# Optimization experiments

Hardware: AMD Instinct MI355X
Metric: run time of the kernel (lower is better)

Reference implementation:

```python
import jax, jax.numpy as jnp
import numpy as np

D = 64          # embed_dim
NH = 4          # nhead
DH = D // NH    # head dim
FF = 2048       # TransformerEncoderLayer default dim_feedforward
V = 1_000_000   # vocab (num items)
MAX_LEN = 50
INSERT_LEN = 10
EPS = 1e-5
N_LAYERS = 2


def setup_inputs() -> dict:
    key = jax.random.key(0)
    ks = jax.random.split(key, 8)
    s = 0.02
    return {
        "ht": jax.random.normal(ks[0], (D,), dtype=jnp.float32),
        "item_emb": jax.random.normal(ks[1], (V, D), dtype=jnp.float32) * s,
        "pos_emb": jax.random.normal(ks[2], (MAX_LEN, D), dtype=jnp.float32) * s,
        "in_proj_w": jax.random.normal(ks[3], (N_LAYERS, 3 * D, D), dtype=jnp.float32) * s,
        "in_proj_b": jnp.zeros((N_LAYERS, 3 * D), jnp.float32),
        "out_w": jax.random.normal(ks[4], (N_LAYERS, D, D), dtype=jnp.float32) * s,
        "out_b": jnp.zeros((N_LAYERS, D), jnp.float32),
        "ln1_w": jnp.ones((N_LAYERS, D), jnp.float32),
        "ln1_b": jnp.zeros((N_LAYERS, D), jnp.float32),
        "ln2_w": jnp.ones((N_LAYERS, D), jnp.float32),
        "ln2_b": jnp.zeros((N_LAYERS, D), jnp.float32),
        "ffn1_w": jax.random.normal(ks[5], (N_LAYERS, FF, D), dtype=jnp.float32) * s,
        "ffn1_b": jnp.zeros((N_LAYERS, FF), jnp.float32),
        "ffn2_w": jax.random.normal(ks[6], (N_LAYERS, D, FF), dtype=jnp.float32) * s,
        "ffn2_b": jnp.zeros((N_LAYERS, D), jnp.float32),
    }


def _ln(x, w, b):
    m = jnp.mean(x, axis=-1, keepdims=True)
    v = jnp.mean(jnp.square(x - m), axis=-1, keepdims=True)
    return (x - m) * jax.lax.rsqrt(v + EPS) * w + b


def _encoder_layer(x, ipw, ipb, ow, ob, l1w, l1b, l2w, l2b, f1w, f1b, f2w, f2b):
    # x: [S, D]; post-norm TransformerEncoderLayer (PyTorch defaults, eval mode)
    S = x.shape[0]
    qkv = x @ ipw.T + ipb                      # [S, 3D]
    q, k, v = jnp.split(qkv, 3, axis=-1)
    q = q.reshape(S, NH, DH)
    k = k.reshape(S, NH, DH)
    v = v.reshape(S, NH, DH)
    scores = jnp.einsum('shd,thd->hst', q, k) / jnp.sqrt(jnp.float32(DH))
    attn = jax.nn.softmax(scores, axis=-1)
    o = jnp.einsum('hst,thd->shd', attn, v).reshape(S, D)
    o = o @ ow.T + ob
    x = _ln(x + o, l1w, l1b)
    ff = jax.nn.relu(x @ f1w.T + f1b) @ f2w.T + f2b
    return _ln(x + ff, l2w, l2b)


def reference(ht, item_emb, pos_emb, in_proj_w, in_proj_b, out_w, out_b,
              ln1_w, ln1_b, ln2_w, ln2_b, ffn1_w, ffn1_b, ffn2_w, ffn2_b):
    gen = []         # generated item indices (traced int scalars)
    logits_all = []
    for _ in range(INSERT_LEN):
        if gen:
            gen_embed = item_emb[jnp.stack(gen)]             # [t, D]
            stack = jnp.concatenate([ht[None, :], gen_embed], axis=0)
        else:
            stack = ht[None, :]
        S = stack.shape[0]
        x = stack + pos_emb[:S]
        for l in range(N_LAYERS):
            x = _encoder_layer(x, in_proj_w[l], in_proj_b[l], out_w[l], out_b[l],
                               ln1_w[l], ln1_b[l], ln2_w[l], ln2_b[l],
                               ffn1_w[l], ffn1_b[l], ffn2_w[l], ffn2_b[l])
        logits = x[-1] @ item_emb.T                           # [V]
        gen.append(jnp.argmax(logits))
        logits_all.append(logits)
    return jnp.stack(logits_all), jnp.stack(gen)
```

## Files before the change

### kernel.cpp

```cpp
#include <hip/hip_runtime.h>

typedef unsigned long long u64;
typedef unsigned int u32;

#define V_ 1000000
#define STEPS_ 10
#define EPS_ 1e-5f
#define MARGIN_ 0.06f
#define FP8_SCALE 2048.0f
#define FP8_INV (1.0f / 2048.0f)
#define NCH 8192
#define CH 123
#define NBLK 64

__device__ __forceinline__ u64 pack_best(float v, int idx) {
    u32 u = __float_as_uint(v);
    u = (u & 0x80000000u) ? ~u : (u | 0x80000000u);
    return ((u64)u << 32) | (u64)(~(u32)idx);
}
__device__ __forceinline__ int unpack_idx(u64 p) { return (int)(~(u32)p); }
__device__ __forceinline__ float unpack_val(u64 p) {
    u32 hi = (u32)(p >> 32);
    return __uint_as_float((hi & 0x80000000u) ? (hi ^ 0x80000000u) : ~hi);
}
__device__ __forceinline__ u64 shfl_xor_u64(u64 v, int m) {
    u32 lo = (u32)v, hi = (u32)(v >> 32);
    lo = (u32)__shfl_xor((int)lo, m);
    hi = (u32)__shfl_xor((int)hi, m);
    return ((u64)hi << 32) | lo;
}

#define FP8_DOT16(u, q, p) do { \
    auto a0 = __builtin_amdgcn_cvt_pk_f32_fp8((u).x, false); \
    auto a1 = __builtin_amdgcn_cvt_pk_f32_fp8((u).x, true);  \
    auto b0 = __builtin_amdgcn_cvt_pk_f32_fp8((u).y, false); \
    auto b1 = __builtin_amdgcn_cvt_pk_f32_fp8((u).y, true);  \
    auto c0 = __builtin_amdgcn_cvt_pk_f32_fp8((u).z, false); \
    auto c1 = __builtin_amdgcn_cvt_pk_f32_fp8((u).z, true);  \
    auto d0 = __builtin_amdgcn_cvt_pk_f32_fp8((u).w, false); \
    auto d1 = __builtin_amdgcn_cvt_pk_f32_fp8((u).w, true);  \
    p = q[0]*a0[0] + q[1]*a0[1] + q[2]*a1[0] + q[3]*a1[1] \
      + q[4]*b0[0] + q[5]*b0[1] + q[6]*b1[0] + q[7]*b1[1] \
      + q[8]*c0[0] + q[9]*c0[1] + q[10]*c1[0] + q[11]*c1[1] \
      + q[12]*d0[0] + q[13]*d0[1] + q[14]*d1[0] + q[15]*d1[1]; \
} while (0)

__device__ __forceinline__ void grid_bar(u32* ctr, u32 expect) {
    __syncthreads();
    if (threadIdx.x == 0) {
        __hip_atomic_fetch_add(ctr, 1u, __ATOMIC_RELEASE, __HIP_MEMORY_SCOPE_AGENT);
        while (__hip_atomic_load(ctr, __ATOMIC_RELAXED, __HIP_MEMORY_SCOPE_AGENT) < expect)
            __builtin_amdgcn_s_sleep(4);
        __builtin_amdgcn_fence(__ATOMIC_ACQUIRE, "agent");
    }
    __syncthreads();
}

__device__ int resolve_argmax(const u64* __restrict__ cand,
                              const u32* __restrict__ emb8,
                              const float* __restrict__ item_emb,
                              const float* __restrict__ y_last,
                              const float* __restrict__ lnw,
                              const float* __restrict__ lnb,
                              float* s_xl, int* s_list, int* s_qg, u64* s_wm,
                              int* s_cnt, int* s_qcnt, u64* s_best)
{
    const int tid = threadIdx.x;
    if (tid < 64) {
        float v = y_last[tid];
        float m = v;
        #pragma unroll
        for (int o = 1; o < 64; o <<= 1) m += __shfl_xor(m, o);
        m *= (1.f / 64.f);
        float df = v - m;
        float var = df * df;
        #pragma unroll
        for (int o = 1; o < 64; o <<= 1) var += __shfl_xor(var, o);
        var *= (1.f / 64.f);
        s_xl[tid] = df * (1.f / sqrtf(var + EPS_)) * lnw[tid] + lnb[tid];
    }
    if (tid == 0) { *s_cnt = 0; *s_qcnt = 0; *s_best = 0ull; }
    __syncthreads();

    u64 m = 0ull;
    for (int i = tid; i < NCH; i += 256) { u64 c = cand[i]; if (c > m) m = c; }
    #pragma unroll
    for (int o = 1; o < 64; o <<= 1) { u64 x = shfl_xor_u64(m, o); if (x > m) m = x; }
    if ((tid & 63) == 0) s_wm[tid >> 6] = m;
    __syncthreads();
    if (tid == 0) {
        u64 b = s_wm[0];
        for (int i = 1; i < 4; i++) if (s_wm[i] > b) b = s_wm[i];
        s_wm[0] = b;
    }
    __syncthreads();
    const float thr = unpack_val(s_wm[0]) - MARGIN_;

    for (int i = tid; i < NCH; i += 256) {
        if (unpack_val(cand[i]) >= thr) {
            int p = atomicAdd(s_qcnt, 1);
            if (p < 64) s_qg[p] = i;
        }
    }
    __syncthreads();
    int nq = *s_qcnt; if (nq > 64) nq = 64;

    {
        const int l4 = tid & 3, rl = tid >> 2;
        float q[16];
        #pragma unroll
        for (int i = 0; i < 16; i++) q[i] = s_xl[l4 * 16 + i] * FP8_INV;
        for (int ci = 0; ci < nq; ci++) {
            const int r0 = s_qg[ci] * CH;
            #pragma unroll
            for (int half = 0; half < 2; half++) {
                int loc = half * 64 + rl;
                int row = r0 + loc;
                if (loc < CH && row < V_) {
                    uint4 u = ((const uint4*)emb8)[(size_t)row * 4 + l4];
                    float p;
                    FP8_DOT16(u, q, p);
                    p += __shfl_xor(p, 1);
                    p += __shfl_xor(p, 2);
                    if (l4 == 0 && p >= thr - 1e-3f) {
                        int pp = atomicAdd(s_cnt, 1);
                        if (pp < 128) s_list[pp] = row;
                    }
                }
            }
        }
    }
    __syncthreads();
    int n = *s_cnt; if (n > 128) n = 128;

    const int wid = tid >> 6, lane = tid & 63;
    for (int c = wid; c < n; c += 4) {
        int row = s_list[c];
        float p = s_xl[lane] * item_emb[(size_t)row * 64 + lane];
        #pragma unroll
        for (int o = 1; o < 64; o <<= 1) p += __shfl_xor(p, o);
        if (lane == 0) atomicMax(s_best, pack_best(p, row));
    }
    __syncthreads();
    return unpack_idx(*s_best);
}

__global__ __launch_bounds__(256) void step_kernel(
    const float* __restrict__ ht, const float* __restrict__ item_emb,
    const float* __restrict__ pos_emb,
    const float* __restrict__ ipw, const float* __restrict__ ipb,
    const float* __restrict__ ow, const float* __restrict__ ob,
    const float* __restrict__ l1w, const float* __restrict__ l1b,
    const float* __restrict__ l2w, const float* __restrict__ l2b,
    const float* __restrict__ f1w, const float* __restrict__ f1b,
    const float* __restrict__ f2w, const float* __restrict__ f2b,
    const u64* __restrict__ cand, const u32* __restrict__ emb8,
    float* __restrict__ y_last,
    int* __restrict__ gen_idx, float* __restrict__ gen_out,
    float* __restrict__ y0, float* __restrict__ hbuf, float* __restrict__ hbuf2,
    u32* __restrict__ bar, int t)
{
    const int S = t + 1;
    const int tid = threadIdx.x, bid = blockIdx.x;
    __shared__ __align__(16) float x[640], qkv[1920], o_[640], y2[640], xps[640];
    __shared__ __align__(16) float xpl[64];
    __shared__ float att[400], rm[10], rr[10], sw[4][10], xl[64], ol[64], y2l[64];
    __shared__ int list[128], qg[64], cnt, qcnt;
    __shared__ u64 wm[4], best;

    const float* ipw1 = ipw + 192 * 64;  const float* ipb1 = ipb + 192;
    const float* ow1  = ow + 64 * 64;    const float* ob1  = ob + 64;
    const float* l1w1 = l1w + 64;        const float* l1b1 = l1b + 64;
    const float* l2w1 = l2w + 64;        const float* l2b1 = l2b + 64;
    const float* f1w1 = f1w + 2048 * 64; const float* f1b1 = f1b + 2048;
    const float* f2w1 = f2w + (size_t)64 * 2048; const float* f2b1 = f2b + 64;

    int newidx = -1;
    if (t > 0) {
        newidx = resolve_argmax(cand, emb8, item_emb, y_last, l2w1, l2b1,
                                xl, list, qg, wm, &cnt, &qcnt, &best);
        if (bid == 0 && tid == 0) { gen_idx[t - 1] = newidx; gen_out[t - 1] = (float)newidx; }
    }
    __syncthreads();

    for (int i = tid; i < S * 64; i += 256) {
        int s = i >> 6, d = i & 63;
        float base;
        if (s == 0) base = ht[d];
        else {
            int gi = (s == t) ? newidx : gen_idx[s - 1];
            base = item_emb[(size_t)gi * 64 + d];
        }
        x[i] = base + pos_emb[i];
    }
    __syncthreads();

    for (int i = tid; i < S * 192; i += 256) {
        int s = i / 192, j2 = i % 192;
        float acc = ipb[j2];
        const float4* wr = (const float4*)(ipw + j2 * 64);
        const float4* xr = (const float4*)(x + s * 64);
        #pragma unroll
        for (int k = 0; k < 16; k++) {
            float4 w4 = wr[k], xv = xr[k];
            acc += w4.x * xv.x + w4.y * xv.y + w4.z * xv.z + w4.w * xv.w;
        }
        qkv[i] = acc;
    }
    __syncthreads();

    for (int i = tid; i < 4 * S * S; i += 256) {
        int h = i / (S * S), r = i % (S * S);
        int si = r / S, ti = r % S;
        const float* qr = qkv + si * 192 + h * 16;
        const float* kr = qkv + ti * 192 + 64 + h * 16;
        float acc = 0.f;
        #pragma unroll
        for (int k = 0; k < 16; k++) acc += qr[k] * kr[k];
        att[(h * S + si) * S + ti] = acc * 0.25f;
    }
    __syncthreads();
    for (int i = tid; i < 4 * S; i += 256) {
        float* row = att + i * S;
        float mx = row[0];
        for (int j2 = 1; j2 < S; j2++) mx = fmaxf(mx, row[j2]);
        float sm = 0.f;
        for (int j2 = 0; j2 < S; j2++) { float e = expf(row[j2] - mx); row[j2] = e; sm += e; }
        float inv = 1.f / sm;
        for (int j2 = 0; j2 < S; j2++) row[j2] *= inv;
    }
    __syncthreads();
    for (int i = tid; i < S * 64; i += 256) {
        int si = i >> 6, d = i & 63, h = d >> 4, dh = d & 15;
        const float* ar = att + (h * S + si) * S;
        float acc = 0.f;
        for (int ti = 0; ti < S; ti++) acc += ar[ti] * qkv[ti * 192 + 128 + h * 16 + dh];
        o_[i] = acc;
    }
    __syncthreads();
    for (int i = tid; i < S * 64; i += 256) {
        int s = i >> 6, d = i & 63;
        float acc = ob[d] + x[i];
        const float4* wr = (const float4*)(ow + d * 64);
        const float4* orow = (const float4*)(o_ + s * 64);
        #pragma unroll
        for (int k = 0; k < 16; k++) {
            float4 w4 = wr[k], ov = orow[k];
            acc += w4.x * ov.x + w4.y * ov.y + w4.z * ov.z + w4.w * ov.w;
        }
        y2[i] = acc;
    }
    __syncthreads();
    if (tid < S) {
        const float* yr = y2 + tid * 64;
        float m = 0.f;
        for (int k = 0; k < 64; k++) m += yr[k];
        m *= (1.f / 64.f);
        float v = 0.f;
        for (int k = 0; k < 64; k++) { float df = yr[k] - m; v += df * df; }
        rm[tid] = m;
        rr[tid] = 1.f / sqrtf(v * (1.f / 64.f) + EPS_);
    }
    __syncthreads();
    for (int i = tid; i < S * 64; i += 256) {
        int s = i >> 6, d = i & 63;
        xps[i] = (y2[i] - rm[s]) * rr[s] * l1w[d] + l1b[d];
    }
    __syncthreads();

    const int jl = tid >> 3, kp = tid & 7;
    const int j = bid * 32 + jl;
    {
        const float4* wr = (const float4*)(f1w + (size_t)j * 64);
        float4 wa = wr[kp * 2], wb = wr[kp * 2 + 1];
        float b1 = f1b[j];
        for (int s = 0; s < S; s++) {
            const float4* xr = (const float4*)(xps + s * 64);
            float4 xa = xr[kp * 2], xb = xr[kp * 2 + 1];
            float p = wa.x * xa.x + wa.y * xa.y + wa.z * xa.z + wa.w * xa.w
                    + wb.x * xb.x + wb.y * xb.y + wb.z * xb.z + wb.w * xb.w;
            p += __shfl_xor(p, 1);
            p += __shfl_xor(p, 2);
            p += __shfl_xor(p, 4);
            if (kp == 0) hbuf[s * 2048 + j] = fmaxf(p + b1, 0.f);
        }
    }
    grid_bar(bar + t * 4 + 0, NBLK);

    {
        const int d = bid;
        const float4* w4 = (const float4*)(f2w + (size_t)d * 2048 + tid * 8);
        float4 w0 = w4[0], w1 = w4[1];
        for (int s = 0; s < S; s++) {
            const float4* h4 = (const float4*)(hbuf + s * 2048 + tid * 8);
            float4 h0 = h4[0], h1 = h4[1];
            float p = w0.x * h0.x + w0.y * h0.y + w0.z * h0.z + w0.w * h0.w
                    + w1.x * h1.x + w1.y * h1.y + w1.z * h1.z + w1.w * h1.w;
            #pragma unroll
            for (int o = 1; o < 64; o <<= 1) p += __shfl_xor(p, o);
            if ((tid & 63) == 0) sw[tid >> 6][s] = p;
        }
        __syncthreads();
        if (tid < S)
            y0[tid * 64 + d] = sw[0][tid] + sw[1][tid] + sw[2][tid] + sw[3][tid]
                             + f2b[d] + xps[tid * 64 + d];
    }
    grid_bar(bar + t * 4 + 1, NBLK);

    for (int i = tid; i < S * 64; i += 256) y2[i] = y0[i];
    __syncthreads();
    if (tid < S) {
        const float* yr = y2 + tid * 64;
        float m = 0.f;
        for (int k = 0; k < 64; k++) m += yr[k];
        m *= (1.f / 64.f);
        float v = 0.f;
        for (int k = 0; k < 64; k++) { float df = yr[k] - m; v += df * df; }
        rm[tid] = m;
        rr[tid] = 1.f / sqrtf(v * (1.f / 64.f) + EPS_);
    }
    __syncthreads();
    for (int i = tid; i < S * 64; i += 256) {
        int s = i >> 6, d = i & 63;
        x[i] = (y2[i] - rm[s]) * rr[s] * l2w[d] + l2b[d];
    }
    __syncthreads();

    for (int i = tid; i < S * 192; i += 256) {
        int s = i / 192, j2 = i % 192;
        float acc = ipb1[j2];
        const float4* wr = (const float4*)(ipw1 + j2 * 64);
        const float4* xr = (const float4*)(x + s * 64);
        #pragma unroll
        for (int k = 0; k < 16; k++) {
            float4 w4 = wr[k], xv = xr[k];
            acc += w4.x * xv.x + w4.y * xv.y + w4.z * xv.z + w4.w * xv.w;
        }
        qkv[i] = acc;
    }
    __syncthreads();

    for (int i = tid; i < 4 * S; i += 256) {
        int h = i / S, ti = i % S;
        const float* qr = qkv + (S - 1) * 192 + h * 16;
        const float* kr = qkv + ti * 192 + 64 + h * 16;
        float acc = 0.f;
        #pragma unroll
        for (int k = 0; k < 16; k++) acc += qr[k] * kr[k];
        att[h * S + ti] = acc * 0.25f;
    }
    __syncthreads();
    if (tid < 4) {
        float* row = att + tid * S;
        float mx = row[0];
        for (int j2 = 1; j2 < S; j2++) mx = fmaxf(mx, row[j2]);
        float sm = 0.f;
        for (int j2 = 0; j2 < S; j2++) { float e = expf(row[j2] - mx); row[j2] = e; sm += e; }
        float inv = 1.f / sm;
        for (int j2 = 0; j2 < S; j2++) row[j2] *= inv;
    }
    __syncthreads();
    if (tid < 64) {
        int h = tid >> 4, dh = tid & 15;
        const float* ar = att + h * S;
        float acc = 0.f;
        for (int ti = 0; ti < S; ti++) acc += ar[ti] * qkv[ti * 192 + 128 + h * 16 + dh];
        ol[tid] = acc;
    }
    __syncthreads();
    if (tid < 64) {
        float acc = ob1[tid] + x[(S - 1) * 64 + tid];
        const float* wr = ow1 + tid * 64;
        for (int k = 0; k < 64; k++) acc += ol[k] * wr[k];
        y2l[tid] = acc;
    }
    __syncthreads();
    if (tid < 64) {
        float v = y2l[tid];
        float m = v;
        #pragma unroll
        for (int o = 1; o < 64; o <<= 1) m += __shfl_xor(m, o);
        m *= (1.f / 64.f);
        float df = v - m;
        float var = df * df;
        #pragma unroll
        for (int o = 1; o < 64; o <<= 1) var += __shfl_xor(var, o);
        float r = 1.f / sqrtf(var * (1.f / 64.f) + EPS_);
        xpl[tid] = df * r * l1w1[tid] + l1b1[tid];
    }
    __syncthreads();

    {
        const float4* wr = (const float4*)(f1w1 + (size_t)j * 64);
        float4 wa = wr[kp * 2], wb = wr[kp * 2 + 1];
        const float4* xr = (const float4*)xpl;
        float4 xa = xr[kp * 2], xb = xr[kp * 2 + 1];
        float p = wa.x * xa.x + wa.y * xa.y + wa.z * xa.z + wa.w * xa.w
                + wb.x * xb.x + wb.y * xb.y + wb.z * xb.z + wb.w * xb.w;
        p += __shfl_xor(p, 1);
        p += __shfl_xor(p, 2);
        p += __shfl_xor(p, 4);
        if (kp == 0) hbuf2[j] = fmaxf(p + f1b1[j], 0.f);
    }
    grid_bar(bar + t * 4 + 2, NBLK);

    {
        const int d = bid;
        const float4* w4 = (const float4*)(f2w1 + (size_t)d * 2048 + tid * 8);
        const float4* h4 = (const float4*)(hbuf2 + tid * 8);
        float4 w0 = w4[0], w1 = w4[1], h0 = h4[0], h1 = h4[1];
        float p = w0.x * h0.x + w0.y * h0.y + w0.z * h0.z + w0.w * h0.w
                + w1.x * h1.x + w1.y * h1.y + w1.z * h1.z + w1.w * h1.w;
        #pragma unroll
        for (int o = 1; o < 64; o <<= 1) p += __shfl_xor(p, o);
        if ((tid & 63) == 0) sw[tid >> 6][0] = p;
        __syncthreads();
        if (tid == 0) y_last[d] = sw[0][0] + sw[1][0] + sw[2][0] + sw[3][0] + f2b1[d] + xpl[d];
    }
}

__global__ __launch_bounds__(256) void scan0_kernel(
    const float* __restrict__ item_emb, const float* __restrict__ y_last,
    const float* __restrict__ lnw, const float* __restrict__ lnb,
    u64* __restrict__ cand, float* __restrict__ xl_all, u32* __restrict__ emb8)
{
    const int tid = threadIdx.x;
    __shared__ float xl[64];
    if (tid < 64) {
        float v = y_last[tid];
        float m = v;
        #pragma unroll
        for (int o = 1; o < 64; o <<= 1) m += __shfl_xor(m, o);
        m *= (1.f / 64.f);
        float df = v - m;
        float var = df * df;
        #pragma unroll
        for (int o = 1; o < 64; o <<= 1) var += __shfl_xor(var, o);
        float r = 1.f / sqrtf(var * (1.f / 64.f) + EPS_);
        float v_ = df * r * lnw[tid] + lnb[tid];
        xl[tid] = v_;
        if (blockIdx.x == 0) xl_all[tid] = v_;
    }
    __syncthreads();

    const int lane = tid & 63, wid = tid >> 6;
    const int g = blockIdx.x * 4 + wid;
    const int l16 = lane & 15, rl = lane >> 4;
    float4 q = ((const float4*)xl)[l16];
    const int r0 = g * CH;
    u64 lb = 0ull;
    for (int it = 0; it < 31; it++) {
        int loc = it * 4 + rl;
        int row = r0 + loc;
        if (loc < CH && row < V_) {
            float4 e = ((const float4*)(item_emb + (size_t)row * 64))[l16];
            u32 pk8 = (u32)__builtin_amdgcn_cvt_pk_fp8_f32(e.x * FP8_SCALE, e.y * FP8_SCALE, 0, false);
            pk8 = (u32)__builtin_amdgcn_cvt_pk_fp8_f32(e.z * FP8_SCALE, e.w * FP8_SCALE, (int)pk8, true);
            emb8[(size_t)row * 16 + l16] = pk8;
            float p = q.x * e.x + q.y * e.y + q.z * e.z + q.w * e.w;
            p += __shfl_xor(p, 1);
            p += __shfl_xor(p, 2);
            p += __shfl_xor(p, 4);
            p += __shfl_xor(p, 8);
            if (l16 == 0) { u64 pk = pack_best(p, row); if (pk > lb) lb = pk; }
        }
    }
    #pragma unroll
    for (int o = 1; o < 64; o <<= 1) { u64 xv = shfl_xor_u64(lb, o); if (xv > lb) lb = xv; }
    if (lane == 0) cand[g] = lb;
}

__global__ __launch_bounds__(256) void scan_fp8_kernel(
    const u32* __restrict__ emb8, const float* __restrict__ y_last,
    const float* __restrict__ lnw, const float* __restrict__ lnb,
    u64* __restrict__ cand, float* __restrict__ xl_all, int t)
{
    const int tid = threadIdx.x;
    __shared__ float xls[64];
    if (tid < 64) {
        float v = y_last[tid];
        float m = v;
        #pragma unroll
        for (int o = 1; o < 64; o <<= 1) m += __shfl_xor(m, o);
        m *= (1.f / 64.f);
        float df = v - m;
        float var = df * df;
        #pragma unroll
        for (int o = 1; o < 64; o <<= 1) var += __shfl_xor(var, o);
        float r = 1.f / sqrtf(var * (1.f / 64.f) + EPS_);
        float v_ = df * r * lnw[tid] + lnb[tid];
        if (blockIdx.x == 0) xl_all[t * 64 + tid] = v_;
        xls[tid] = v_ * FP8_INV;
    }
    __syncthreads();

    const int lane = tid & 63, wid = tid >> 6;
    const int g = blockIdx.x * 4 + wid;
    const int l4 = lane & 3, rl = lane >> 2;
    float q[16];
    #pragma unroll
    for (int i = 0; i < 16; i++) q[i] = xls[l4 * 16 + i];
    const int r0 = g * CH;
    u64 lb = 0ull;
    for (int it = 0; it < 8; it++) {
        int loc = it * 16 + rl;
        int row = r0 + loc;
        if (loc < CH && row < V_) {
            uint4 u = ((const uint4*)emb8)[(size_t)row * 4 + l4];
            float p;
            FP8_DOT16(u, q, p);
            p += __shfl_xor(p, 1);
            p += __shfl_xor(p, 2);
            if (l4 == 0) { u64 pk = pack_best(p, row); if (pk > lb) lb = pk; }
        }
    }
    #pragma unroll
    for (int o = 1; o < 64; o <<= 1) { u64 xv = shfl_xor_u64(lb, o); if (xv > lb) lb = xv; }
    if (lane == 0) cand[g] = lb;
}

__global__ __launch_bounds__(256) void finalize_kernel(
    const u64* __restrict__ cand, const u32* __restrict__ emb8,
    const float* __restrict__ item_emb, const float* __restrict__ y_last,
    const float* __restrict__ lnw, const float* __restrict__ lnb,
    float* __restrict__ gen_out)
{
    __shared__ float xl[64];
    __shared__ int list[128], qg[64], cnt, qcnt;
    __shared__ u64 wm[4], best;
    int r = resolve_argmax(cand, emb8, item_emb, y_last, lnw, lnb,
                           xl, list, qg, wm, &cnt, &qcnt, &best);
    if (threadIdx.x == 0) gen_out[STEPS_ - 1] = (float)r;
}

__global__ __launch_bounds__(256) void logits_all_kernel(
    const float* __restrict__ item_emb, const float* __restrict__ xl_all,
    float* __restrict__ out)
{
    const int tid = threadIdx.x;
    const int lane = tid & 63, wv = tid >> 6;
    const int l4 = lane & 3, qd = lane >> 2;

    float4 qv[10][4];
    #pragma unroll
    for (int p = 0; p < 10; p++) {
        #pragma unroll
        for (int c = 0; c < 4; c++)
            qv[p][c] = *(const float4*)(xl_all + p * 64 + l4 * 16 + c * 4);
    }

    const int row_in_blk = wv * 16 + qd;
    for (int tile = blockIdx.x; tile < V_ / 64; tile += gridDim.x) {
        const int row = tile * 64 + row_in_blk;
        const float4* er = (const float4*)(item_emb + (size_t)row * 64 + l4 * 16);
        float4 e0 = er[0], e1 = er[1], e2 = er[2], e3 = er[3];
        float acc[10];
        #pragma unroll
        for (int p = 0; p < 10; p++) {
            float s = qv[p][0].x*e0.x + qv[p][0].y*e0.y + qv[p][0].z*e0.z + qv[p][0].w*e0.w
                    + qv[p][1].x*e1.x + qv[p][1].y*e1.y + qv[p][1].z*e1.z + qv[p][1].w*e1.w
                    + qv[p][2].x*e2.x + qv[p][2].y*e2.y + qv[p][2].z*e2.z + qv[p][2].w*e2.w
                    + qv[p][3].x*e3.x + qv[p][3].y*e3.y + qv[p][3].z*e3.z + qv[p][3].w*e3.w;
            s += __shfl_xor(s, 1);
            s += __shfl_xor(s, 2);
            acc[p] = s;
        }
        if (l4 == 0) {
            #pragma unroll
            for (int p = 0; p < 10; p++)
                out[(size_t)p * V_ + row] = acc[p];
        }
    }
}

extern "C" void kernel_launch(void* const* d_in, const int* in_sizes, int n_in,
                              void* d_out, int out_size, void* d_ws, size_t ws_size,
                              hipStream_t stream) {
    const float* ht       = (const float*)d_in[0];
    const float* item_emb = (const float*)d_in[1];
    const float* pos_emb  = (const float*)d_in[2];
    const float* ipw      = (const float*)d_in[3];
    const float* ipb      = (const float*)d_in[4];
    const float* ow       = (const float*)d_in[5];
    const float* ob       = (const float*)d_in[6];
    const float* l1w      = (const float*)d_in[7];
    const float* l1b      = (const float*)d_in[8];
    const float* l2w      = (const float*)d_in[9];
    const float* l2b      = (const float*)d_in[10];
    const float* f1w      = (const float*)d_in[11];
    const float* f1b      = (const float*)d_in[12];
    const float* f2w      = (const float*)d_in[13];
    const float* f2b      = (const float*)d_in[14];

    float* out = (float*)d_out;
    char* ws = (char*)d_ws;
    int*   gen_idx = (int*)ws;
    float* y_last  = (float*)(ws + 64);
    float* y0      = (float*)(ws + 512);
    float* hbuf2   = (float*)(ws + 3072);
    float* xl_all  = (float*)(ws + 11264);
    u32*   bar     = (u32*)(ws + 14336);
    float* hbuf    = (float*)(ws + 16384);
    u64*   cand    = (u64*)(ws + 131072);
    u32*   emb8    = (u32*)(ws + 262144);
    float* gen_out = out + (size_t)STEPS_ * V_;

    hipMemsetAsync(bar, 0, 256, stream);

    for (int t = 0; t < STEPS_; t++) {
        step_kernel<<<NBLK, 256, 0, stream>>>(
            ht, item_emb, pos_emb, ipw, ipb, ow, ob, l1w, l1b, l2w, l2b,
            f1w, f1b, f2w, f2b, cand, emb8, y_last, gen_idx, gen_out,
            y0, hbuf, hbuf2, bar, t);
        if (t == 0)
            scan0_kernel<<<2048, 256, 0, stream>>>(
                item_emb, y_last, l2w + 64, l2b + 64, cand, xl_all, emb8);
        else
            scan_fp8_kernel<<<2048, 256, 0, stream>>>(
                emb8, y_last, l2w + 64, l2b + 64, cand, xl_all, t);
    }
    finalize_kernel<<<1, 256, 0, stream>>>(
        cand, emb8, item_emb, y_last, l2w + 64, l2b + 64, gen_out);
    logits_all_kernel<<<2048, 256, 0, stream>>>(item_emb, xl_all, out);
}
```

Baseline: 1.177 ms.

## Replace 64-block grid-barrier step kernel with single 1024-thread block templated on length

```diff
diff --git a/kernel.cpp b/kernel.cpp
--- a/kernel.cpp
+++ b/kernel.cpp
@@ -11,7 +11,7 @@
 #define FP8_INV (1.0f / 2048.0f)
 #define NCH 8192
 #define CH 123
-#define NBLK 64
+#define NTH 1024
 
 __device__ __forceinline__ u64 pack_best(float v, int idx) {
     u32 u = __float_as_uint(v);
@@ -45,17 +45,6 @@
       + q[12]*d0[0] + q[13]*d0[1] + q[14]*d1[0] + q[15]*d1[1]; \
 } while (0)
 
-__device__ __forceinline__ void grid_bar(u32* ctr, u32 expect) {
-    __syncthreads();
-    if (threadIdx.x == 0) {
-        __hip_atomic_fetch_add(ctr, 1u, __ATOMIC_RELEASE, __HIP_MEMORY_SCOPE_AGENT);
-        while (__hip_atomic_load(ctr, __ATOMIC_RELAXED, __HIP_MEMORY_SCOPE_AGENT) < expect)
-            __builtin_amdgcn_s_sleep(4);
-        __builtin_amdgcn_fence(__ATOMIC_ACQUIRE, "agent");
-    }
-    __syncthreads();
-}
-
 __device__ int resolve_argmax(const u64* __restrict__ cand,
                               const u32* __restrict__ emb8,
                               const float* __restrict__ item_emb,
@@ -83,20 +72,20 @@
     __syncthreads();
 
     u64 m = 0ull;
-    for (int i = tid; i < NCH; i += 256) { u64 c = cand[i]; if (c > m) m = c; }
+    for (int i = tid; i < NCH; i += NTH) { u64 c = cand[i]; if (c > m) m = c; }
     #pragma unroll
     for (int o = 1; o < 64; o <<= 1) { u64 x = shfl_xor_u64(m, o); if (x > m) m = x; }
     if ((tid & 63) == 0) s_wm[tid >> 6] = m;
     __syncthreads();
     if (tid == 0) {
         u64 b = s_wm[0];
-        for (int i = 1; i < 4; i++) if (s_wm[i] > b) b = s_wm[i];
+        for (int i = 1; i < NTH / 64; i++) if (s_wm[i] > b) b = s_wm[i];
         s_wm[0] = b;
     }
     __syncthreads();
     const float thr = unpack_val(s_wm[0]) - MARGIN_;
 
-    for (int i = tid; i < NCH; i += 256) {
+    for (int i = tid; i < NCH; i += NTH) {
         if (unpack_val(cand[i]) >= thr) {
             int p = atomicAdd(s_qcnt, 1);
             if (p < 64) s_qg[p] = i;
@@ -111,21 +100,16 @@
         #pragma unroll
         for (int i = 0; i < 16; i++) q[i] = s_xl[l4 * 16 + i] * FP8_INV;
         for (int ci = 0; ci < nq; ci++) {
-            const int r0 = s_qg[ci] * CH;
-            #pragma unroll
-            for (int half = 0; half < 2; half++) {
-                int loc = half * 64 + rl;
-                int row = r0 + loc;
-                if (loc < CH && row < V_) {
-                    uint4 u = ((const uint4*)emb8)[(size_t)row * 4 + l4];
-                    float p;
-                    FP8_DOT16(u, q, p);
-                    p += __shfl_xor(p, 1);
-                    p += __shfl_xor(p, 2);
-                    if (l4 == 0 && p >= thr - 1e-3f) {
-                        int pp = atomicAdd(s_cnt, 1);
-                        if (pp < 128) s_list[pp] = row;
-                    }
+            int row = s_qg[ci] * CH + rl;
+            if (rl < CH && row < V_) {
+                uint4 u = ((const uint4*)emb8)[(size_t)row * 4 + l4];
+                float p;
+                FP8_DOT16(u, q, p);
+                p += __shfl_xor(p, 1);
+                p += __shfl_xor(p, 2);
+                if (l4 == 0 && p >= thr - 1e-3f) {
+                    int pp = atomicAdd(s_cnt, 1);
+                    if (pp < 128) s_list[pp] = row;
                 }
             }
         }
@@ -134,7 +118,7 @@
     int n = *s_cnt; if (n > 128) n = 128;
 
     const int wid = tid >> 6, lane = tid & 63;
-    for (int c = wid; c < n; c += 4) {
+    for (int c = wid; c < n; c += NTH / 64) {
         int row = s_list[c];
         float p = s_xl[lane] * item_emb[(size_t)row * 64 + lane];
         #pragma unroll
@@ -145,7 +129,8 @@
     return unpack_idx(*s_best);
 }
 
-__global__ __launch_bounds__(256) void step_kernel(
+template<int SS>
+__global__ __launch_bounds__(NTH) void step1_kernel(
     const float* __restrict__ ht, const float* __restrict__ item_emb,
     const float* __restrict__ pos_emb,
     const float* __restrict__ ipw, const float* __restrict__ ipb,
@@ -155,18 +140,19 @@
     const float* __restrict__ f1w, const float* __restrict__ f1b,
     const float* __restrict__ f2w, const float* __restrict__ f2b,
     const u64* __restrict__ cand, const u32* __restrict__ emb8,
-    float* __restrict__ y_last,
-    int* __restrict__ gen_idx, float* __restrict__ gen_out,
-    float* __restrict__ y0, float* __restrict__ hbuf, float* __restrict__ hbuf2,
-    u32* __restrict__ bar, int t)
+    float* __restrict__ y_last, int* __restrict__ gen_idx,
+    float* __restrict__ gen_out)
 {
-    const int S = t + 1;
-    const int tid = threadIdx.x, bid = blockIdx.x;
-    __shared__ __align__(16) float x[640], qkv[1920], o_[640], y2[640], xps[640];
-    __shared__ __align__(16) float xpl[64];
-    __shared__ float att[400], rm[10], rr[10], sw[4][10], xl[64], ol[64], y2l[64];
+    const int t = SS - 1;
+    const int tid = threadIdx.x;
+    const int lane = tid & 63, wv = tid >> 6;
+    __shared__ __align__(16) float x[SS * 64], qkv[SS * 192], o_[SS * 64];
+    __shared__ __align__(16) float y2[SS * 64], xps[SS * 64];
+    __shared__ __align__(16) float xpl[64], hb2[2048];
+    __shared__ __align__(16) float hb[SS * 2048];
+    __shared__ float att[4 * SS * SS], rm[SS], rr[SS], xl[64], ol[64], y2l[64];
     __shared__ int list[128], qg[64], cnt, qcnt;
-    __shared__ u64 wm[4], best;
+    __shared__ u64 wm[NTH / 64], best;
 
     const float* ipw1 = ipw + 192 * 64;  const float* ipb1 = ipb + 192;
     const float* ow1  = ow + 64 * 64;    const float* ob1  = ob + 64;
@@ -176,26 +162,23 @@
     const float* f2w1 = f2w + (size_t)64 * 2048; const float* f2b1 = f2b + 64;
 
     int newidx = -1;
-    if (t > 0) {
+    if constexpr (SS > 1) {
         newidx = resolve_argmax(cand, emb8, item_emb, y_last, l2w1, l2b1,
                                 xl, list, qg, wm, &cnt, &qcnt, &best);
-        if (bid == 0 && tid == 0) { gen_idx[t - 1] = newidx; gen_out[t - 1] = (float)newidx; }
-    }
-    __syncthreads();
-
-    for (int i = tid; i < S * 64; i += 256) {
-        int s = i >> 6, d = i & 63;
+        if (tid == 0) { gen_idx[t - 1] = newidx; gen_out[t - 1] = (float)newidx; }
+    }
+    __syncthreads();
+
+    if (tid < SS * 64) {
+        int s = tid >> 6, d = tid & 63;
         float base;
         if (s == 0) base = ht[d];
-        else {
-            int gi = (s == t) ? newidx : gen_idx[s - 1];
-            base = item_emb[(size_t)gi * 64 + d];
-        }
-        x[i] = base + pos_emb[i];
-    }
-    __syncthreads();
-
-    for (int i = tid; i < S * 192; i += 256) {
+        else base = item_emb[(size_t)((s == t) ? newidx : gen_idx[s - 1]) * 64 + d];
+        x[tid] = base + pos_emb[tid];
+    }
+    __syncthreads();
+
+    for (int i = tid; i < SS * 192; i += NTH) {
         int s = i / 192, j2 = i % 192;
         float acc = ipb[j2];
         const float4* wr = (const float4*)(ipw + j2 * 64);
@@ -209,38 +192,42 @@
     }
     __syncthreads();
 
-    for (int i = tid; i < 4 * S * S; i += 256) {
-        int h = i / (S * S), r = i % (S * S);
-        int si = r / S, ti = r % S;
+    if (tid < 4 * SS * SS) {
+        int h = tid / (SS * SS), r = tid % (SS * SS);
+        int si = r / SS, ti = r % SS;
         const float* qr = qkv + si * 192 + h * 16;
         const float* kr = qkv + ti * 192 + 64 + h * 16;
         float acc = 0.f;
         #pragma unroll
         for (int k = 0; k < 16; k++) acc += qr[k] * kr[k];
-        att[(h * S + si) * S + ti] = acc * 0.25f;
-    }
-    __syncthreads();
-    for (int i = tid; i < 4 * S; i += 256) {
-        float* row = att + i * S;
+        att[(h * SS + si) * SS + ti] = acc * 0.25f;
+    }
+    __syncthreads();
+    if (tid < 4 * SS) {
+        float* row = att + tid * SS;
         float mx = row[0];
-        for (int j2 = 1; j2 < S; j2++) mx = fmaxf(mx, row[j2]);
+        #pragma unroll
+        for (int j2 = 1; j2 < SS; j2++) mx = fmaxf(mx, row[j2]);
         float sm = 0.f;
-        for (int j2 = 0; j2 < S; j2++) { float e = expf(row[j2] - mx); row[j2] = e; sm += e; }
+        #pragma unroll
+        for (int j2 = 0; j2 < SS; j2++) { float e = expf(row[j2] - mx); row[j2] = e; sm += e; }
         float inv = 1.f / sm;
-        for (int j2 = 0; j2 < S; j2++) row[j2] *= inv;
-    }
-    __syncthreads();
-    for (int i = tid; i < S * 64; i += 256) {
-        int si = i >> 6, d = i & 63, h = d >> 4, dh = d & 15;
-        const float* ar = att + (h * S + si) * S;
+        #pragma unroll
+        for (int j2 = 0; j2 < SS; j2++) row[j2] *= inv;
+    }
+    __syncthreads();
+    if (tid < SS * 64) {
+        int si = tid >> 6, d = tid & 63, h = d >> 4, dh = d & 15;
+        const float* ar = att + (h * SS + si) * SS;
         float acc = 0.f;
-        for (int ti = 0; ti < S; ti++) acc += ar[ti] * qkv[ti * 192 + 128 + h * 16 + dh];
-        o_[i] = acc;
-    }
-    __syncthreads();
-    for (int i = tid; i < S * 64; i += 256) {
-        int s = i >> 6, d = i & 63;
-        float acc = ob[d] + x[i];
+        #pragma unroll
+        for (int ti = 0; ti < SS; ti++) acc += ar[ti] * qkv[ti * 192 + 128 + h * 16 + dh];
+        o_[tid] = acc;
+    }
+    __syncthreads();
+    if (tid < SS * 64) {
+        int s = tid >> 6, d = tid & 63;
+        float acc = ob[d] + x[tid];
         const float4* wr = (const float4*)(ow + d * 64);
         const float4* orow = (const float4*)(o_ + s * 64);
         #pragma unroll
@@ -248,10 +235,10 @@
             float4 w4 = wr[k], ov = orow[k];
             acc += w4.x * ov.x + w4.y * ov.y + w4.z * ov.z + w4.w * ov.w;
         }
-        y2[i] = acc;
-    }
-    __syncthreads();
-    if (tid < S) {
+        y2[tid] = acc;
+    }
+    __syncthreads();
+    if (tid < SS) {
         const float* yr = y2 + tid * 64;
         float m = 0.f;
         for (int k = 0; k < 64; k++) m += yr[k];
@@ -262,54 +249,76 @@
         rr[tid] = 1.f / sqrtf(v * (1.f / 64.f) + EPS_);
     }
     __syncthreads();
-    for (int i = tid; i < S * 64; i += 256) {
-        int s = i >> 6, d = i & 63;
-        xps[i] = (y2[i] - rm[s]) * rr[s] * l1w[d] + l1b[d];
-    }
-    __syncthreads();
-
-    const int jl = tid >> 3, kp = tid & 7;
-    const int j = bid * 32 + jl;
+    if (tid < SS * 64) {
+        int s = tid >> 6, d = tid & 63;
+        xps[tid] = (y2[tid] - rm[s]) * rr[s] * l1w[d] + l1b[d];
+    }
+    __syncthreads();
+
     {
-        const float4* wr = (const float4*)(f1w + (size_t)j * 64);
-        float4 wa = wr[kp * 2], wb = wr[kp * 2 + 1];
-        float b1 = f1b[j];
-        for (int s = 0; s < S; s++) {
-            const float4* xr = (const float4*)(xps + s * 64);
-            float4 xa = xr[kp * 2], xb = xr[kp * 2 + 1];
-            float p = wa.x * xa.x + wa.y * xa.y + wa.z * xa.z + wa.w * xa.w
-                    + wb.x * xb.x + wb.y * xb.y + wb.z * xb.z + wb.w * xb.w;
-            p += __shfl_xor(p, 1);
-            p += __shfl_xor(p, 2);
-            p += __shfl_xor(p, 4);
-            if (kp == 0) hbuf[s * 2048 + j] = fmaxf(p + b1, 0.f);
-        }
-    }
-    grid_bar(bar + t * 4 + 0, NBLK);
+        const int jl = tid >> 3, kp = tid & 7;
+        #pragma unroll 1
+        for (int jg = 0; jg < 16; jg++) {
+            int j = jg * 128 + jl;
+            const float4* wr = (const float4*)(f1w + (size_t)j * 64);
+            float4 wa = wr[kp * 2], wb = wr[kp * 2 + 1];
+            float b1 = f1b[j];
+            #pragma unroll
+            for (int s = 0; s < SS; s++) {
+                const float4* xr = (const float4*)(xps + s * 64);
+                float4 xa = xr[kp * 2], xb = xr[kp * 2 + 1];
+                float p = wa.x * xa.x + wa.y * xa.y + wa.z * xa.z + wa.w * xa.w
+                        + wb.x * xb.x + wb.y * xb.y + wb.z * xb.z + wb.w * xb.w;
+                p += __shfl_xor(p, 1);
+                p += __shfl_xor(p, 2);
+                p += __shfl_xor(p, 4);
+                if (kp == 0) hb[s * 2048 + j] = fmaxf(p + b1, 0.f);
+            }
+        }
+    }
+    __syncthreads();
 
     {
-        const int d = bid;
-        const float4* w4 = (const float4*)(f2w + (size_t)d * 2048 + tid * 8);
-        float4 w0 = w4[0], w1 = w4[1];
-        for (int s = 0; s < S; s++) {
-            const float4* h4 = (const float4*)(hbuf + s * 2048 + tid * 8);
-            float4 h0 = h4[0], h1 = h4[1];
-            float p = w0.x * h0.x + w0.y * h0.y + w0.z * h0.z + w0.w * h0.w
-                    + w1.x * h1.x + w1.y * h1.y + w1.z * h1.z + w1.w * h1.w;
+        const int d0 = wv * 4;
+        float a[4][SS];
+        #pragma unroll
+        for (int di = 0; di < 4; di++)
             #pragma unroll
-            for (int o = 1; o < 64; o <<= 1) p += __shfl_xor(p, o);
-            if ((tid & 63) == 0) sw[tid >> 6][s] = p;
-        }
-        __syncthreads();
-        if (tid < S)
-            y0[tid * 64 + d] = sw[0][tid] + sw[1][tid] + sw[2][tid] + sw[3][tid]
-                             + f2b[d] + xps[tid * 64 + d];
-    }
-    grid_bar(bar + t * 4 + 1, NBLK);
-
-    for (int i = tid; i < S * 64; i += 256) y2[i] = y0[i];
-    __syncthreads();
-    if (tid < S) {
+            for (int s = 0; s < SS; s++) a[di][s] = 0.f;
+        #pragma unroll 2
+        for (int k = 0; k < 32; k++) {
+            int jj = k * 64 + lane;
+            float w0 = f2w[(size_t)(d0 + 0) * 2048 + jj];
+            float w1 = f2w[(size_t)(d0 + 1) * 2048 + jj];
+            float w2 = f2w[(size_t)(d0 + 2) * 2048 + jj];
+            float w3 = f2w[(size_t)(d0 + 3) * 2048 + jj];
+            #pragma unroll
+            for (int s = 0; s < SS; s++) {
+                float hv = hb[s * 2048 + jj];
+                a[0][s] += w0 * hv; a[1][s] += w1 * hv;
+                a[2][s] += w2 * hv; a[3][s] += w3 * hv;
+            }
+        }
+        #pragma unroll
+        for (int o = 1; o < 64; o <<= 1)
+            #pragma unroll
+            for (int di = 0; di < 4; di++)
+                #pragma unroll
+                for (int s = 0; s < SS; s++)
+                    a[di][s] += __shfl_xor(a[di][s], o);
+        if (lane == 0) {
+            #pragma unroll
+            for (int di = 0; di < 4; di++)
+                #pragma unroll
+                for (int s = 0; s < SS; s++)
+                    o_[s * 64 + d0 + di] = a[di][s];
+        }
+    }
+    __syncthreads();
+
+    if (tid < SS * 64) y2[tid] = o_[tid] + f2b[tid & 63] + xps[tid];
+    __syncthreads();
+    if (tid < SS) {
         const float* yr = y2 + tid * 64;
         float m = 0.f;
         for (int k = 0; k < 64; k++) m += yr[k];
@@ -320,13 +329,13 @@
         rr[tid] = 1.f / sqrtf(v * (1.f / 64.f) + EPS_);
     }
     __syncthreads();
-    for (int i = tid; i < S * 64; i += 256) {
-        int s = i >> 6, d = i & 63;
-        x[i] = (y2[i] - rm[s]) * rr[s] * l2w[d] + l2b[d];
-    }
-    __syncthreads();
-
-    for (int i = tid; i < S * 192; i += 256) {
+    if (tid < SS * 64) {
+        int s = tid >> 6, d = tid & 63;
+        x[tid] = (y2[tid] - rm[s]) * rr[s] * l2w[d] + l2b[d];
+    }
+    __syncthreads();
+
+    for (int i = tid; i < SS * 192; i += NTH) {
         int s = i / 192, j2 = i % 192;
         float acc = ipb1[j2];
         const float4* wr = (const float4*)(ipw1 + j2 * 64);
@@ -340,36 +349,40 @@
     }
     __syncthreads();
 
-    for (int i = tid; i < 4 * S; i += 256) {
-        int h = i / S, ti = i % S;
-        const float* qr = qkv + (S - 1) * 192 + h * 16;
+    if (tid < 4 * SS) {
+        int h = tid / SS, ti = tid % SS;
+        const float* qr = qkv + (SS - 1) * 192 + h * 16;
         const float* kr = qkv + ti * 192 + 64 + h * 16;
         float acc = 0.f;
         #pragma unroll
         for (int k = 0; k < 16; k++) acc += qr[k] * kr[k];
-        att[h * S + ti] = acc * 0.25f;
+        att[h * SS + ti] = acc * 0.25f;
     }
     __syncthreads();
     if (tid < 4) {
-        float* row = att + tid * S;
+        float* row = att + tid * SS;
         float mx = row[0];
-        for (int j2 = 1; j2 < S; j2++) mx = fmaxf(mx, row[j2]);
+        #pragma unroll
+        for (int j2 = 1; j2 < SS; j2++) mx = fmaxf(mx, row[j2]);
         float sm = 0.f;
-        for (int j2 = 0; j2 < S; j2++) { float e = expf(row[j2] - mx); row[j2] = e; sm += e; }
+        #pragma unroll
+        for (int j2 = 0; j2 < SS; j2++) { float e = expf(row[j2] - mx); row[j2] = e; sm += e; }
         float inv = 1.f / sm;
-        for (int j2 = 0; j2 < S; j2++) row[j2] *= inv;
+        #pragma unroll
+        for (int j2 = 0; j2 < SS; j2++) row[j2] *= inv;
     }
     __syncthreads();
     if (tid < 64) {
         int h = tid >> 4, dh = tid & 15;
-        const float* ar = att + h * S;
+        const float* ar = att + h * SS;
         float acc = 0.f;
-        for (int ti = 0; ti < S; ti++) acc += ar[ti] * qkv[ti * 192 + 128 + h * 16 + dh];
+        #pragma unroll
+        for (int ti = 0; ti < SS; ti++) acc += ar[ti] * qkv[ti * 192 + 128 + h * 16 + dh];
         ol[tid] = acc;
     }
     __syncthreads();
     if (tid < 64) {
-        float acc = ob1[tid] + x[(S - 1) * 64 + tid];
+        float acc = ob1[tid] + x[(SS - 1) * 64 + tid];
         const float* wr = ow1 + tid * 64;
         for (int k = 0; k < 64; k++) acc += ol[k] * wr[k];
         y2l[tid] = acc;
@@ -391,31 +404,47 @@
     __syncthreads();
 
     {
-        const float4* wr = (const float4*)(f1w1 + (size_t)j * 64);
-        float4 wa = wr[kp * 2], wb = wr[kp * 2 + 1];
+        const int jl = tid >> 3, kp = tid & 7;
         const float4* xr = (const float4*)xpl;
         float4 xa = xr[kp * 2], xb = xr[kp * 2 + 1];
-        float p = wa.x * xa.x + wa.y * xa.y + wa.z * xa.z + wa.w * xa.w
-                + wb.x * xb.x + wb.y * xb.y + wb.z * xb.z + wb.w * xb.w;
-        p += __shfl_xor(p, 1);
-        p += __shfl_xor(p, 2);
-        p += __shfl_xor(p, 4);
-        if (kp == 0) hbuf2[j] = fmaxf(p + f1b1[j], 0.f);
-    }
-    grid_bar(bar + t * 4 + 2, NBLK);
+        #pragma unroll 1
+        for (int jg = 0; jg < 16; jg++) {
+            int j = jg * 128 + jl;
+            const float4* wr = (const float4*)(f1w1 + (size_t)j * 64);
+            float4 wa = wr[kp * 2], wb = wr[kp * 2 + 1];
+            float p = wa.x * xa.x + wa.y * xa.y + wa.z * xa.z + wa.w * xa.w
+                    + wb.x * xb.x + wb.y * xb.y + wb.z * xb.z + wb.w * xb.w;
+            p += __shfl_xor(p, 1);
+            p += __shfl_xor(p, 2);
+            p += __shfl_xor(p, 4);
+            if (kp == 0) hb2[j] = fmaxf(p + f1b1[j], 0.f);
+        }
+    }
+    __syncthreads();
 
     {
-        const int d = bid;
-        const float4* w4 = (const float4*)(f2w1 + (size_t)d * 2048 + tid * 8);
-        const float4* h4 = (const float4*)(hbuf2 + tid * 8);
-        float4 w0 = w4[0], w1 = w4[1], h0 = h4[0], h1 = h4[1];
-        float p = w0.x * h0.x + w0.y * h0.y + w0.z * h0.z + w0.w * h0.w
-                + w1.x * h1.x + w1.y * h1.y + w1.z * h1.z + w1.w * h1.w;
-        #pragma unroll
-        for (int o = 1; o < 64; o <<= 1) p += __shfl_xor(p, o);
-        if ((tid & 63) == 0) sw[tid >> 6][0] = p;
-        __syncthreads();
-        if (tid == 0) y_last[d] = sw[0][0] + sw[1][0] + sw[2][0] + sw[3][0] + f2b1[d] + xpl[d];
+        const int d0 = wv * 4;
+        float a0 = 0.f, a1 = 0.f, a2 = 0.f, a3 = 0.f;
+        #pragma unroll 2
+        for (int k = 0; k < 32; k++) {
+            int jj = k * 64 + lane;
+            float hv = hb2[jj];
+            a0 += f2w1[(size_t)(d0 + 0) * 2048 + jj] * hv;
+            a1 += f2w1[(size_t)(d0 + 1) * 2048 + jj] * hv;
+            a2 += f2w1[(size_t)(d0 + 2) * 2048 + jj] * hv;
+            a3 += f2w1[(size_t)(d0 + 3) * 2048 + jj] * hv;
+        }
+        #pragma unroll
+        for (int o = 1; o < 64; o <<= 1) {
+            a0 += __shfl_xor(a0, o); a1 += __shfl_xor(a1, o);
+            a2 += __shfl_xor(a2, o); a3 += __shfl_xor(a3, o);
+        }
+        if (lane == 0) {
+            y_last[d0 + 0] = a0 + f2b1[d0 + 0] + xpl[d0 + 0];
+            y_last[d0 + 1] = a1 + f2b1[d0 + 1] + xpl[d0 + 1];
+            y_last[d0 + 2] = a2 + f2b1[d0 + 2] + xpl[d0 + 2];
+            y_last[d0 + 3] = a3 + f2b1[d0 + 3] + xpl[d0 + 3];
+        }
     }
 }
 
@@ -467,6 +496,11 @@
     }
     #pragma unroll
     for (int o = 1; o < 64; o <<= 1) { u64 xv = shfl_xor_u64(lb, o); if (xv > lb) lb = xv; }
+    __shared__ u64 sb[4];
+    if (lane == 0) sb[wid] = lb;
+    __syncthreads();
+    if (tid == 0) {
+    }
     if (lane == 0) cand[g] = lb;
 }
 
@@ -519,7 +553,7 @@
     if (lane == 0) cand[g] = lb;
 }
 
-__global__ __launch_bounds__(256) void finalize_kernel(
+__global__ __launch_bounds__(NTH) void finalize_kernel(
     const u64* __restrict__ cand, const u32* __restrict__ emb8,
     const float* __restrict__ item_emb, const float* __restrict__ y_last,
     const float* __restrict__ lnw, const float* __restrict__ lnb,
@@ -527,7 +561,7 @@
 {
     __shared__ float xl[64];
     __shared__ int list[128], qg[64], cnt, qcnt;
-    __shared__ u64 wm[4], best;
+    __shared__ u64 wm[NTH / 64], best;
     int r = resolve_argmax(cand, emb8, item_emb, y_last, lnw, lnb,
                            xl, list, qg, wm, &cnt, &qcnt, &best);
     if (threadIdx.x == 0) gen_out[STEPS_ - 1] = (float)r;
@@ -596,22 +630,27 @@
     char* ws = (char*)d_ws;
     int*   gen_idx = (int*)ws;
     float* y_last  = (float*)(ws + 64);
-    float* y0      = (float*)(ws + 512);
-    float* hbuf2   = (float*)(ws + 3072);
     float* xl_all  = (float*)(ws + 11264);
-    u32*   bar     = (u32*)(ws + 14336);
-    float* hbuf    = (float*)(ws + 16384);
     u64*   cand    = (u64*)(ws + 131072);
     u32*   emb8    = (u32*)(ws + 262144);
     float* gen_out = out + (size_t)STEPS_ * V_;
 
-    hipMemsetAsync(bar, 0, 256, stream);
+#define STEP_ARGS ht, item_emb, pos_emb, ipw, ipb, ow, ob, l1w, l1b, l2w, l2b, \
+                  f1w, f1b, f2w, f2b, cand, emb8, y_last, gen_idx, gen_out
 
     for (int t = 0; t < STEPS_; t++) {
-        step_kernel<<<NBLK, 256, 0, stream>>>(
-            ht, item_emb, pos_emb, ipw, ipb, ow, ob, l1w, l1b, l2w, l2b,
-            f1w, f1b, f2w, f2b, cand, emb8, y_last, gen_idx, gen_out,
-            y0, hbuf, hbuf2, bar, t);
+        switch (t) {
+            case 0: step1_kernel<1><<<1, NTH, 0, stream>>>(STEP_ARGS); break;
+            case 1: step1_kernel<2><<<1, NTH, 0, stream>>>(STEP_ARGS); break;
+            case 2: step1_kernel<3><<<1, NTH, 0, stream>>>(STEP_ARGS); break;
+            case 3: step1_kernel<4><<<1, NTH, 0, stream>>>(STEP_ARGS); break;
+            case 4: step1_kernel<5><<<1, NTH, 0, stream>>>(STEP_ARGS); break;
+            case 5: step1_kernel<6><<<1, NTH, 0, stream>>>(STEP_ARGS); break;
+            case 6: step1_kernel<7><<<1, NTH, 0, stream>>>(STEP_ARGS); break;
+            case 7: step1_kernel<8><<<1, NTH, 0, stream>>>(STEP_ARGS); break;
+            case 8: step1_kernel<9><<<1, NTH, 0, stream>>>(STEP_ARGS); break;
+            case 9: step1_kernel<10><<<1, NTH, 0, stream>>>(STEP_ARGS); break;
+        }
         if (t == 0)
             scan0_kernel<<<2048, 256, 0, stream>>>(
                 item_emb, y_last, l2w + 64, l2b + 64, cand, xl_all, emb8);
@@ -619,7 +658,7 @@
             scan_fp8_kernel<<<2048, 256, 0, stream>>>(
                 emb8, y_last, l2w + 64, l2b + 64, cand, xl_all, t);
     }
-    finalize_kernel<<<1, 256, 0, stream>>>(
+    finalize_kernel<<<1, NTH, 0, stream>>>(
         cand, emb8, item_emb, y_last, l2w + 64, l2b + 64, gen_out);
     logits_all_kernel<<<2048, 256, 0, stream>>>(item_emb, xl_all, out);
 }
```

Result: slower. 1.434 ms (+21.9%).
